# Performance work log

Measured on AMD Instinct MI355X. Metric: run time of the kernel, lower is better.

Reference implementation:

```python
import jax, jax.numpy as jnp
import numpy as np

N_NODES = 100000


def gcn_layer(x, row, col, ew, W, b, n_nodes):
    # PyG GCNConv: add self-loops (weight 1), symmetric normalization
    # deg^{-1/2}[row] * w * deg^{-1/2}[col], linear transform, scatter-add to col.
    loop = jnp.arange(n_nodes, dtype=row.dtype)
    row_f = jnp.concatenate([row, loop])
    col_f = jnp.concatenate([col, loop])
    ew_f = jnp.concatenate([ew, jnp.ones((n_nodes,), dtype=ew.dtype)])
    deg = jax.ops.segment_sum(ew_f, col_f, num_segments=n_nodes)  # [N]
    dinv = jnp.where(deg > 0, jax.lax.rsqrt(deg), 0.0)
    norm = dinv[row_f] * ew_f * dinv[col_f]  # [E+N]
    h = x @ W  # [N, F_out]
    msg = norm[:, None] * h[row_f]  # [E+N, F_out]
    out = jax.ops.segment_sum(msg, col_f, num_segments=n_nodes)
    return out + b


def setup_inputs() -> dict:
    key = jax.random.key(0)
    ks = jax.random.split(key, 6)
    n, e, d_in, d_h = N_NODES, 3200000, 128, 16
    x = jax.random.normal(ks[0], (n, d_in), dtype=jnp.float32)
    edge_index = jax.random.randint(ks[1], (2, e), 0, n, dtype=jnp.int64)
    edge_weight = jax.random.uniform(ks[2], (e,), dtype=jnp.float32)
    W1 = jax.random.normal(ks[3], (d_in, d_h), dtype=jnp.float32) * (1.0 / np.sqrt(d_in))
    b1 = jnp.zeros((d_h,), dtype=jnp.float32)
    W2 = jax.random.normal(ks[4], (d_h, 1), dtype=jnp.float32) * (1.0 / np.sqrt(d_h))
    b2 = jnp.zeros((1,), dtype=jnp.float32)
    return {"x": x, "edge_index": edge_index, "edge_weight": edge_weight,
            "W1": W1, "b1": b1, "W2": W2, "b2": b2}


def reference(x, edge_index, edge_weight, W1, b1, W2, b2):
    row, col = edge_index[0], edge_index[1]
    n = x.shape[0]
    h = gcn_layer(x, row, col, edge_weight, W1, b1, n)
    h = jax.nn.relu(h)
    out = gcn_layer(h, row, col, edge_weight, W2, b2, n)
    return out.squeeze(-1)  # [N]
```

## Files before the change

### kernel.cpp

```cpp
#include <hip/hip_runtime.h>
#include <hip/hip_bf16.h>


#define DH 16
#define BSH 6
#define BNODES 64
#define NB_MAX 1568
#define CHUNK 4096
#define HCHUNK 8192
#define NSLICE 4
#define SE_CAP 768
#define SE2_CAP 1280

#define BFL(u) __uint_as_float((u) << 16)
#define BFH(u) __uint_as_float((u) & 0xFFFF0000u)

typedef unsigned int u32x2 __attribute__((ext_vector_type(2)));

static __device__ __forceinline__ uint2 ntload_u2(const uint2* p) {
    u32x2 v = __builtin_nontemporal_load((const u32x2*)p);
    return make_uint2(v.x, v.y);
}
static __device__ __forceinline__ uint agent_load_u32(const uint* p) {
    return __hip_atomic_load((uint*)p, __ATOMIC_RELAXED, __HIP_MEMORY_SCOPE_AGENT);
}
static __device__ __forceinline__ ushort agent_load_u16(const ushort* p) {
    return __hip_atomic_load((ushort*)p, __ATOMIC_RELAXED, __HIP_MEMORY_SCOPE_AGENT);
}

__global__ __launch_bounds__(256) void k_Ahist(const int* __restrict__ col,
                                               int* __restrict__ gCnt, int E, int NB) {
    __shared__ int lh[NB_MAX];
    const int tid = threadIdx.x;
    for (int i = tid; i < NB; i += 256) lh[i] = 0;
    __syncthreads();
    const int base = blockIdx.x * HCHUNK;
    #pragma unroll
    for (int k = 0; k < 32; ++k) {
        int e = base + tid + 256 * k;
        if (e < E) atomicAdd(&lh[col[e] >> BSH], 1);
    }
    __syncthreads();
    for (int i = tid; i < NB; i += 256) {
        int v = lh[i];
        if (v) atomicAdd(&gCnt[i], v);
    }
}

__global__ __launch_bounds__(1024) void k_Ascan(const int* __restrict__ gCnt,
                                                int* __restrict__ gBase,
                                                int* __restrict__ gCursor,
                                                int NB, int E) {
    __shared__ int s[1024];
    const int t = threadIdx.x;
    const int i0 = 2 * t, i1 = 2 * t + 1;
    int a = (i0 < NB) ? gCnt[i0] : 0;
    int b = (i1 < NB) ? gCnt[i1] : 0;
    int v = a + b;
    s[t] = v;
    __syncthreads();
    for (int off = 1; off < 1024; off <<= 1) {
        int u = (t >= off) ? s[t - off] : 0;
        __syncthreads();
        s[t] += u;
        __syncthreads();
    }
    int ex = s[t] - v;
    if (i0 < NB) { gBase[i0] = ex;     gCursor[i0] = ex; }
    if (i1 < NB) { gBase[i1] = ex + a; gCursor[i1] = ex + a; }
    if (t == 0) gBase[NB] = E;
}

__global__ __launch_bounds__(256) void k_Ascatter(const int* __restrict__ row,
                                                  const int* __restrict__ col,
                                                  const float* __restrict__ ew,
                                                  int* __restrict__ gCursor,
                                                  uint2* __restrict__ edata,
                                                  int E, int NB) {
    __shared__ int lh[NB_MAX];
    __shared__ int lbase[NB_MAX];
    __shared__ int lcur[NB_MAX];
    __shared__ int tsum[256];
    __shared__ unsigned short sbuck[CHUNK];
    __shared__ uint2 stage[CHUNK];
    const int tid = threadIdx.x;
    for (int i = tid; i < NB; i += 256) lh[i] = 0;
    __syncthreads();
    const int base = blockIdx.x * CHUNK;
    int r_[16], c_[16];
    float w_[16];
    #pragma unroll
    for (int k = 0; k < 16; ++k) {
        int e = base + tid + 256 * k;
        bool ok = e < E;
        c_[k] = ok ? col[e] : -1;
        r_[k] = ok ? row[e] : 0;
        w_[k] = ok ? ew[e] : 0.f;
        if (ok) atomicAdd(&lh[c_[k] >> BSH], 1);
    }
    __syncthreads();
    const int t0 = tid * 8;
    int c8[8];
    int mysum = 0;
    #pragma unroll
    for (int k = 0; k < 8; ++k) {
        c8[k] = (t0 + k < NB) ? lh[t0 + k] : 0;
        mysum += c8[k];
    }
    tsum[tid] = mysum;
    __syncthreads();
    for (int off = 1; off < 256; off <<= 1) {
        int u = (tid >= off) ? tsum[tid - off] : 0;
        __syncthreads();
        tsum[tid] += u;
        __syncthreads();
    }
    int p = tsum[tid] - mysum;
    #pragma unroll
    for (int k = 0; k < 8; ++k) {
        if (t0 + k < NB) { lbase[t0 + k] = p; lcur[t0 + k] = p; }
        p += c8[k];
    }
    __syncthreads();
    for (int b = tid; b < NB; b += 256) {
        int cnt = lh[b];
        if (cnt) {
            int g = atomicAdd(&gCursor[b], cnt);
            lh[b] = g - lbase[b];
        }
    }
    __syncthreads();
    #pragma unroll
    for (int k = 0; k < 16; ++k) {
        if (c_[k] >= 0) {
            int b = c_[k] >> BSH;
            unsigned rem = (unsigned)(c_[k] & (BNODES - 1));
            int sp = atomicAdd(&lcur[b], 1);
            stage[sp] = make_uint2((unsigned)r_[k] | (rem << 20), __float_as_uint(w_[k]));
            sbuck[sp] = (unsigned short)b;
        }
    }
    __syncthreads();
    int nE = E - base;
    if (nE > CHUNK) nE = CHUNK;
    for (int j = tid; j < nE; j += 256)
        edata[lh[sbuck[j]] + j] = stage[j];
}

__global__ __launch_bounds__(256) void k_deg(const int* __restrict__ gBase,
                                             const uint2* __restrict__ edata,
                                             float* __restrict__ deg, int N) {
    __shared__ float dg[BNODES];
    const int tid = threadIdx.x;
    if (tid < BNODES) dg[tid] = 0.f;
    __syncthreads();
    const int b = blockIdx.x;
    const int s = gBase[b], e = gBase[b + 1];
    for (int i = s + blockIdx.y * 256 + tid; i < e; i += 512) {
        uint2 ed = ntload_u2(&edata[i]);
        atomicAdd(&dg[ed.x >> 20], __uint_as_float(ed.y));
    }
    __syncthreads();
    int node = (b << BSH) + tid;
    if (tid < BNODES && node < N && dg[tid] != 0.f)
        atomicAdd(&deg[node], dg[tid]);
}

__global__ __launch_bounds__(256) void k_h1(const float* __restrict__ x,
                                            const float* __restrict__ W1,
                                            const float* __restrict__ deg,
                                            float* __restrict__ dinv,
                                            __hip_bfloat16* __restrict__ hdb) {
    __shared__ float Ws[128 * DH];
    __shared__ float xs[16 * 132];
    const int t = threadIdx.x;
    const int node0 = blockIdx.x * 16;
    #pragma unroll
    for (int i = 0; i < 8; ++i) Ws[t + 256 * i] = W1[t + 256 * i];
    const float4* xg = (const float4*)(x + (size_t)node0 * 128);
    #pragma unroll
    for (int it = 0; it < 2; ++it) {
        int idx = t + 256 * it;
        int n = idx >> 5, k4 = idx & 31;
        float4 v = xg[n * 32 + k4];
        *(float4*)(&xs[n * 132 + k4 * 4]) = v;
    }
    __syncthreads();
    const int node = t >> 4, feat = t & 15;
    const float* xr = &xs[node * 132];
    float acc = 0.f;
    #pragma unroll 8
    for (int k = 0; k < 128; ++k) acc += xr[k] * Ws[k * DH + feat];
    const int v = node0 + node;
    const float di = rsqrtf(deg[v] + 1.0f);
    if (feat == 0) dinv[v] = di;
    hdb[(size_t)v * DH + feat] = __float2bfloat16(di * acc);
}

__global__ __launch_bounds__(256) void k_gather1(
    const int* __restrict__ gBase, const uint2* __restrict__ edata,
    const __hip_bfloat16* __restrict__ hdb, float* __restrict__ partial) {
    __shared__ float acc[BNODES][DH + 1];
    __shared__ uint2 se[SE_CAP];
    const int tid = threadIdx.x;
    for (int i = tid; i < BNODES * (DH + 1); i += 256) ((float*)acc)[i] = 0.f;
    const int b = blockIdx.x, sl = blockIdx.y;
    const int s = gBase[b], e = gBase[b + 1];
    const int L = e - s;
    const int per = (L + NSLICE - 1) / NSLICE;
    const int s0 = s + sl * per;
    const int e0 = (s0 + per < e) ? (s0 + per) : e;
    const int g = tid >> 3;
    const int f2 = tid & 7;
    const uint* __restrict__ hp = (const uint*)hdb;

    for (int c0 = s0; c0 < e0; c0 += SE_CAP) {
        const int len = ((e0 - c0) < SE_CAP) ? (e0 - c0) : SE_CAP;
        __syncthreads();
        for (int j = tid; j < len; j += 256) se[j] = ntload_u2(&edata[c0 + j]);
        __syncthreads();
        const int nfull = len & ~255;
        for (int j0 = 0; j0 < nfull; j0 += 256) {
            uint2 ed[8];
            uint hv[8];
            #pragma unroll
            for (int k = 0; k < 8; ++k) ed[k] = se[j0 + g + k * 32];
            #pragma unroll
            for (int k = 0; k < 8; ++k)
                hv[k] = agent_load_u32(&hp[(size_t)(ed[k].x & 0xFFFFFu) * 8 + f2]);
            #pragma unroll
            for (int k = 0; k < 8; ++k) {
                const float w = __uint_as_float(ed[k].y);
                const int rem = ed[k].x >> 20;
                atomicAdd(&acc[rem][2 * f2],     w * BFL(hv[k]));
                atomicAdd(&acc[rem][2 * f2 + 1], w * BFH(hv[k]));
            }
        }
        for (int j = nfull + g; j < len; j += 32) {
            const uint2 ed = se[j];
            const uint hv = agent_load_u32(&hp[(size_t)(ed.x & 0xFFFFFu) * 8 + f2]);
            const float w = __uint_as_float(ed.y);
            const int rem = ed.x >> 20;
            atomicAdd(&acc[rem][2 * f2],     w * BFL(hv));
            atomicAdd(&acc[rem][2 * f2 + 1], w * BFH(hv));
        }
    }
    __syncthreads();
    float* ps = partial + ((size_t)b * NSLICE + sl) * (DH * BNODES);
    for (int i = tid; i < DH * BNODES; i += 256)
        ps[i] = acc[i >> 4][i & 15];
}

__global__ __launch_bounds__(256) void k_fin1(
    const float* __restrict__ partial, const float* __restrict__ dinv,
    const __hip_bfloat16* __restrict__ hdb, const float* __restrict__ b1,
    const float* __restrict__ W2, const float* __restrict__ b2,
    __hip_bfloat16* __restrict__ qb, float* __restrict__ out, int N) {
    __shared__ float acc[BNODES][DH + 1];
    __shared__ float b1s[DH], W2s[DH];
    const int tid = threadIdx.x;
    if (tid < DH) { b1s[tid] = b1[tid]; W2s[tid] = W2[tid]; }
    const int b = blockIdx.x;
    const float* ps = partial + (size_t)b * NSLICE * (DH * BNODES);
    for (int i = tid; i < DH * BNODES; i += 256) {
        float s = 0.f;
        #pragma unroll
        for (int sl = 0; sl < NSLICE; ++sl) s += ps[sl * (DH * BNODES) + i];
        acc[i >> 4][i & 15] = s;
    }
    __syncthreads();
    int node = (b << BSH) + tid;
    if (tid < BNODES && node < N) {
        float dc = dinv[node];
        const __hip_bfloat16* hs = hdb + (size_t)node * DH;
        float t = 0.f;
        #pragma unroll
        for (int f = 0; f < DH; ++f) {
            float hv = __bfloat162float(hs[f]);
            t += fmaxf(dc * (acc[tid][f] + hv) + b1s[f], 0.f) * W2s[f];
        }
        float qq = dc * t;
        qb[node] = __float2bfloat16(qq);
        out[node] = b2[0] + dc * qq;
    }
}

__global__ __launch_bounds__(256) void k_gather2(
    const int* __restrict__ gBase, const uint2* __restrict__ edata,
    const float* __restrict__ dinv, const __hip_bfloat16* __restrict__ qb,
    float* __restrict__ out, int N) {
    __shared__ float a2[BNODES];
    __shared__ uint2 se[SE2_CAP];
    const int tid = threadIdx.x;
    if (tid < BNODES) a2[tid] = 0.f;
    const int b = blockIdx.x;
    const int s = gBase[b], e = gBase[b + 1];
    const int L = e - s;
    const int per = (L + 1) >> 1;
    const int s0 = s + blockIdx.y * per;
    const int e0 = (s0 + per < e) ? (s0 + per) : e;
    const ushort* __restrict__ qp = (const ushort*)qb;

    for (int c0 = s0; c0 < e0; c0 += SE2_CAP) {
        const int len = ((e0 - c0) < SE2_CAP) ? (e0 - c0) : SE2_CAP;
        __syncthreads();
        for (int j = tid; j < len; j += 256) se[j] = ntload_u2(&edata[c0 + j]);
        __syncthreads();
        const int nfull = len & ~1023;
        for (int j0 = 0; j0 < nfull; j0 += 1024) {
            uint2 ed[4];
            uint qv[4];
            #pragma unroll
            for (int k = 0; k < 4; ++k) ed[k] = se[j0 + tid + k * 256];
            #pragma unroll
            for (int k = 0; k < 4; ++k)
                qv[k] = (uint)agent_load_u16(&qp[ed[k].x & 0xFFFFFu]);
            #pragma unroll
            for (int k = 0; k < 4; ++k)
                atomicAdd(&a2[ed[k].x >> 20],
                          __uint_as_float(ed[k].y) * __uint_as_float(qv[k] << 16));
        }
        for (int j = nfull + tid; j < len; j += 256) {
            const uint2 ed = se[j];
            const float q = __uint_as_float((uint)agent_load_u16(&qp[ed.x & 0xFFFFFu]) << 16);
            atomicAdd(&a2[ed.x >> 20], __uint_as_float(ed.y) * q);
        }
    }
    __syncthreads();
    int node = (b << BSH) + tid;
    if (tid < BNODES && node < N && a2[tid] != 0.f)
        atomicAdd(&out[node], dinv[node] * a2[tid]);
}

extern "C" void kernel_launch(void* const* d_in, const int* in_sizes, int n_in,
                              void* d_out, int out_size, void* d_ws, size_t ws_size,
                              hipStream_t stream) {
    const float* x  = (const float*)d_in[0];
    const int*   ei = (const int*)d_in[1];
    const float* ew = (const float*)d_in[2];
    const float* W1 = (const float*)d_in[3];
    const float* b1 = (const float*)d_in[4];
    const float* W2 = (const float*)d_in[5];
    const float* b2 = (const float*)d_in[6];
    float* out = (float*)d_out;

    const int N = in_sizes[0] / 128;
    const int E = in_sizes[2];
    const int* row = ei;
    const int* col = ei + E;
    const int NB = (N + BNODES - 1) >> BSH;
    const int NBp = (NB + 3) & ~3;

    int* gCnt    = (int*)d_ws;
    float* deg   = (float*)(gCnt + NBp);
    int* gBase   = (int*)(deg + N);
    int* gCursor = gBase + NBp;
    float* dinv  = (float*)(gCursor + NBp);
    __hip_bfloat16* hdb = (__hip_bfloat16*)(dinv + N);
    __hip_bfloat16* qb  = hdb + (size_t)16 * N;
    uintptr_t pp = (uintptr_t)(qb + N);
    pp = (pp + 15) & ~(uintptr_t)15;
    float* partial = (float*)pp;
    uintptr_t ep = (uintptr_t)(partial + (size_t)NB * NSLICE * (DH * BNODES));
    ep = (ep + 15) & ~(uintptr_t)15;
    uint2* edata = (uint2*)ep;

    const int hblocks = (E + HCHUNK - 1) / HCHUNK;
    const int sblocks = (E + CHUNK - 1) / CHUNK;

    hipMemsetAsync(gCnt, 0, ((size_t)NBp + N) * sizeof(int), stream);
    k_Ahist<<<hblocks, 256, 0, stream>>>(col, gCnt, E, NB);
    k_Ascan<<<1, 1024, 0, stream>>>(gCnt, gBase, gCursor, NB, E);
    k_Ascatter<<<sblocks, 256, 0, stream>>>(row, col, ew, gCursor, edata, E, NB);
    k_deg<<<dim3(NB, 2), 256, 0, stream>>>(gBase, edata, deg, N);
    k_h1<<<N / 16, 256, 0, stream>>>(x, W1, deg, dinv, hdb);
    k_gather1<<<dim3(NB, NSLICE), 256, 0, stream>>>(gBase, edata, hdb, partial);
    k_fin1<<<NB, 256, 0, stream>>>(partial, dinv, hdb, b1, W2, b2, qb, out, N);
    k_gather2<<<dim3(NB, 2), 256, 0, stream>>>(gBase, edata, dinv, qb, out, N);
}
```

Baseline: 532.5 us.

## Replace random feature gathers with row-bucketed scatter into edge-ordered buffers

Adds a second histogram and scatter that bucket edges by source row and record each edge's slot in the col-sorted order. Source features are then pushed from per-block shared memory into an edge-ordered buffer (he16, qe), so the gather kernels read contiguously instead of doing random per-edge loads of h and q. This adds an extra scatter pass, extra workspace of roughly 32 bytes per edge, and possibly several phases when workspace is limited. A fallback path keeps the old algorithm, with plain loads replacing agent-scope atomic loads.

```diff
diff --git a/kernel.cpp b/kernel.cpp
--- a/kernel.cpp
+++ b/kernel.cpp
@@ -8,9 +8,11 @@
 #define NB_MAX 1568
 #define CHUNK 4096
 #define HCHUNK 8192
-#define NSLICE 4
+#define NSL 2
+#define NSL_FB 4
 #define SE_CAP 768
 #define SE2_CAP 1280
+#define HESLACK 65536
 
 #define BFL(u) __uint_as_float((u) << 16)
 #define BFH(u) __uint_as_float((u) & 0xFFFF0000u)
@@ -21,11 +23,31 @@
     u32x2 v = __builtin_nontemporal_load((const u32x2*)p);
     return make_uint2(v.x, v.y);
 }
-static __device__ __forceinline__ uint agent_load_u32(const uint* p) {
-    return __hip_atomic_load((uint*)p, __ATOMIC_RELAXED, __HIP_MEMORY_SCOPE_AGENT);
-}
-static __device__ __forceinline__ ushort agent_load_u16(const ushort* p) {
-    return __hip_atomic_load((ushort*)p, __ATOMIC_RELAXED, __HIP_MEMORY_SCOPE_AGENT);
+
+
+__global__ __launch_bounds__(256) void k_hist2(const int* __restrict__ row,
+                                               const int* __restrict__ col,
+                                               int* __restrict__ gCnt,
+                                               int* __restrict__ rCnt, int E, int NB) {
+    __shared__ int lc[NB_MAX];
+    __shared__ int lr[NB_MAX];
+    const int tid = threadIdx.x;
+    for (int i = tid; i < NB; i += 256) { lc[i] = 0; lr[i] = 0; }
+    __syncthreads();
+    const int base = blockIdx.x * HCHUNK;
+    #pragma unroll
+    for (int k = 0; k < 32; ++k) {
+        int e = base + tid + 256 * k;
+        if (e < E) {
+            atomicAdd(&lc[col[e] >> BSH], 1);
+            atomicAdd(&lr[row[e] >> BSH], 1);
+        }
+    }
+    __syncthreads();
+    for (int i = tid; i < NB; i += 256) {
+        if (lc[i]) atomicAdd(&gCnt[i], lc[i]);
+        if (lr[i]) atomicAdd(&rCnt[i], lr[i]);
+    }
 }
 
 __global__ __launch_bounds__(256) void k_Ahist(const int* __restrict__ col,
@@ -47,15 +69,15 @@
     }
 }
 
-__global__ __launch_bounds__(1024) void k_Ascan(const int* __restrict__ gCnt,
-                                                int* __restrict__ gBase,
-                                                int* __restrict__ gCursor,
+__global__ __launch_bounds__(1024) void k_Ascan(const int* __restrict__ cnt,
+                                                int* __restrict__ basep,
+                                                int* __restrict__ cursor,
                                                 int NB, int E) {
     __shared__ int s[1024];
     const int t = threadIdx.x;
     const int i0 = 2 * t, i1 = 2 * t + 1;
-    int a = (i0 < NB) ? gCnt[i0] : 0;
-    int b = (i1 < NB) ? gCnt[i1] : 0;
+    int a = (i0 < NB) ? cnt[i0] : 0;
+    int b = (i1 < NB) ? cnt[i1] : 0;
     int v = a + b;
     s[t] = v;
     __syncthreads();
@@ -66,9 +88,9 @@
         __syncthreads();
     }
     int ex = s[t] - v;
-    if (i0 < NB) { gBase[i0] = ex;     gCursor[i0] = ex; }
-    if (i1 < NB) { gBase[i1] = ex + a; gCursor[i1] = ex + a; }
-    if (t == 0) gBase[NB] = E;
+    if (i0 < NB) { basep[i0] = ex;     cursor[i0] = ex; }
+    if (i1 < NB) { basep[i1] = ex + a; cursor[i1] = ex + a; }
+    if (t == 0) basep[NB] = E;
 }
 
 __global__ __launch_bounds__(256) void k_Ascatter(const int* __restrict__ row,
@@ -76,6 +98,7 @@
                                                   const float* __restrict__ ew,
                                                   int* __restrict__ gCursor,
                                                   uint2* __restrict__ edata,
+                                                  int* __restrict__ pos,
                                                   int E, int NB) {
     __shared__ int lh[NB_MAX];
     __shared__ int lbase[NB_MAX];
@@ -138,6 +161,7 @@
             int sp = atomicAdd(&lcur[b], 1);
             stage[sp] = make_uint2((unsigned)r_[k] | (rem << 20), __float_as_uint(w_[k]));
             sbuck[sp] = (unsigned short)b;
+            if (pos != nullptr) pos[base + tid + 256 * k] = lh[b] + sp;
         }
     }
     __syncthreads();
@@ -145,6 +169,80 @@
     if (nE > CHUNK) nE = CHUNK;
     for (int j = tid; j < nE; j += 256)
         edata[lh[sbuck[j]] + j] = stage[j];
+}
+
+__global__ __launch_bounds__(256) void k_Rscatter(const int* __restrict__ row,
+                                                  const int* __restrict__ pos,
+                                                  int* __restrict__ rCursor,
+                                                  uint* __restrict__ rrec,
+                                                  int E, int NB) {
+    __shared__ int lh[NB_MAX];
+    __shared__ int lbase[NB_MAX];
+    __shared__ int lcur[NB_MAX];
+    __shared__ int tsum[256];
+    __shared__ unsigned short sbuck[CHUNK];
+    __shared__ uint stage[CHUNK];
+    const int tid = threadIdx.x;
+    for (int i = tid; i < NB; i += 256) lh[i] = 0;
+    __syncthreads();
+    const int base = blockIdx.x * CHUNK;
+    int r_[16];
+    uint p_[16];
+    #pragma unroll
+    for (int k = 0; k < 16; ++k) {
+        int e = base + tid + 256 * k;
+        bool ok = e < E;
+        r_[k] = ok ? row[e] : -1;
+        p_[k] = ok ? (uint)pos[e] : 0u;
+        if (ok) atomicAdd(&lh[r_[k] >> BSH], 1);
+    }
+    __syncthreads();
+    const int t0 = tid * 8;
+    int c8[8];
+    int mysum = 0;
+    #pragma unroll
+    for (int k = 0; k < 8; ++k) {
+        c8[k] = (t0 + k < NB) ? lh[t0 + k] : 0;
+        mysum += c8[k];
+    }
+    tsum[tid] = mysum;
+    __syncthreads();
+    for (int off = 1; off < 256; off <<= 1) {
+        int u = (tid >= off) ? tsum[tid - off] : 0;
+        __syncthreads();
+        tsum[tid] += u;
+        __syncthreads();
+    }
+    int p = tsum[tid] - mysum;
+    #pragma unroll
+    for (int k = 0; k < 8; ++k) {
+        if (t0 + k < NB) { lbase[t0 + k] = p; lcur[t0 + k] = p; }
+        p += c8[k];
+    }
+    __syncthreads();
+    for (int bb = tid; bb < NB; bb += 256) {
+        int cnt = lh[bb];
+        if (cnt) {
+            int g = atomicAdd(&rCursor[bb], cnt);
+            lh[bb] = g - lbase[bb];
+        }
+    }
+    __syncthreads();
+    #pragma unroll
+    for (int k = 0; k < 16; ++k) {
+        if (r_[k] >= 0) {
+            int bb = r_[k] >> BSH;
+            uint rem = (uint)(r_[k] & (BNODES - 1));
+            int sp = atomicAdd(&lcur[bb], 1);
+            stage[sp] = p_[k] | (rem << 26);
+            sbuck[sp] = (unsigned short)bb;
+        }
+    }
+    __syncthreads();
+    int nE = E - base;
+    if (nE > CHUNK) nE = CHUNK;
+    for (int j = tid; j < nE; j += 256)
+        rrec[lh[sbuck[j]] + j] = stage[j];
 }
 
 __global__ __launch_bounds__(256) void k_deg(const int* __restrict__ gBase,
@@ -197,75 +295,101 @@
     hdb[(size_t)v * DH + feat] = __float2bfloat16(di * acc);
 }
 
-__global__ __launch_bounds__(256) void k_gather1(
+
+__global__ __launch_bounds__(256) void k_hgather(const int* __restrict__ rBase,
+                                                 const uint* __restrict__ rrec,
+                                                 const uint* __restrict__ hdb32,
+                                                 uint4* __restrict__ he16, int N,
+                                                 const int* __restrict__ gBase,
+                                                 int bLo, int bHi, int heCap) {
+    __shared__ uint hs[BNODES * 8];
+    const int tid = threadIdx.x;
+    const int b = blockIdx.x;
+    const int slotLo = gBase[bLo], slotHi = gBase[bHi];
+    const int lim = N * 8 - b * 512;
+    for (int i = tid; i < 512; i += 256)
+        hs[i] = (i < lim) ? hdb32[(size_t)b * 512 + i] : 0u;
+    __syncthreads();
+    const int r0 = rBase[b], r1 = rBase[b + 1];
+    for (int j = r0 + blockIdx.y * 256 + tid; j < r1; j += 512) {
+        uint rec = rrec[j];
+        int p = (int)(rec & 0x03FFFFFFu);
+        if (p >= slotLo && p < slotHi) {
+            int q = p - slotLo;
+            if (q < heCap) {
+                const uint* hr = &hs[(rec >> 26) * 8];
+                he16[(size_t)2 * q]     = make_uint4(hr[0], hr[1], hr[2], hr[3]);
+                he16[(size_t)2 * q + 1] = make_uint4(hr[4], hr[5], hr[6], hr[7]);
+            }
+        }
+    }
+}
+
+__global__ __launch_bounds__(256) void k_gather1_p(
     const int* __restrict__ gBase, const uint2* __restrict__ edata,
-    const __hip_bfloat16* __restrict__ hdb, float* __restrict__ partial) {
+    const uint4* __restrict__ he16, float* __restrict__ partial,
+    int bLo, int heCap) {
     __shared__ float acc[BNODES][DH + 1];
-    __shared__ uint2 se[SE_CAP];
     const int tid = threadIdx.x;
     for (int i = tid; i < BNODES * (DH + 1); i += 256) ((float*)acc)[i] = 0.f;
-    const int b = blockIdx.x, sl = blockIdx.y;
+    __syncthreads();
+    const int b = bLo + blockIdx.x, sl = blockIdx.y;
+    const int slotLo = gBase[bLo];
     const int s = gBase[b], e = gBase[b + 1];
     const int L = e - s;
-    const int per = (L + NSLICE - 1) / NSLICE;
+    const int per = (L + NSL - 1) / NSL;
     const int s0 = s + sl * per;
     const int e0 = (s0 + per < e) ? (s0 + per) : e;
-    const int g = tid >> 3;
-    const int f2 = tid & 7;
-    const uint* __restrict__ hp = (const uint*)hdb;
-
-    for (int c0 = s0; c0 < e0; c0 += SE_CAP) {
-        const int len = ((e0 - c0) < SE_CAP) ? (e0 - c0) : SE_CAP;
-        __syncthreads();
-        for (int j = tid; j < len; j += 256) se[j] = ntload_u2(&edata[c0 + j]);
-        __syncthreads();
-        const int nfull = len & ~255;
-        for (int j0 = 0; j0 < nfull; j0 += 256) {
-            uint2 ed[8];
-            uint hv[8];
-            #pragma unroll
-            for (int k = 0; k < 8; ++k) ed[k] = se[j0 + g + k * 32];
-            #pragma unroll
-            for (int k = 0; k < 8; ++k)
-                hv[k] = agent_load_u32(&hp[(size_t)(ed[k].x & 0xFFFFFu) * 8 + f2]);
-            #pragma unroll
-            for (int k = 0; k < 8; ++k) {
-                const float w = __uint_as_float(ed[k].y);
-                const int rem = ed[k].x >> 20;
-                atomicAdd(&acc[rem][2 * f2],     w * BFL(hv[k]));
-                atomicAdd(&acc[rem][2 * f2 + 1], w * BFH(hv[k]));
-            }
-        }
-        for (int j = nfull + g; j < len; j += 32) {
-            const uint2 ed = se[j];
-            const uint hv = agent_load_u32(&hp[(size_t)(ed.x & 0xFFFFFu) * 8 + f2]);
-            const float w = __uint_as_float(ed.y);
-            const int rem = ed.x >> 20;
-            atomicAdd(&acc[rem][2 * f2],     w * BFL(hv));
-            atomicAdd(&acc[rem][2 * f2 + 1], w * BFH(hv));
-        }
-    }
-    __syncthreads();
-    float* ps = partial + ((size_t)b * NSLICE + sl) * (DH * BNODES);
+    const int hf = tid & 1, f0 = hf * 8;
+    for (int jb = s0; jb < e0; jb += 256) {
+        const int j0 = jb + (tid >> 1);
+        const int j1 = j0 + 128;
+        const bool v0 = (j0 < e0) && (j0 - slotLo < heCap);
+        const bool v1 = (j1 < e0) && (j1 - slotLo < heCap);
+        uint4 h0 = v0 ? he16[(size_t)2 * (j0 - slotLo) + hf] : make_uint4(0, 0, 0, 0);
+        uint4 h1 = v1 ? he16[(size_t)2 * (j1 - slotLo) + hf] : make_uint4(0, 0, 0, 0);
+        uint2 d0 = v0 ? edata[j0] : make_uint2(0u, 0u);
+        uint2 d1 = v1 ? edata[j1] : make_uint2(0u, 0u);
+        {
+            const float w = __uint_as_float(d0.y);
+            float* a = &acc[d0.x >> 20][f0];
+            atomicAdd(a + 0, w * BFL(h0.x)); atomicAdd(a + 1, w * BFH(h0.x));
+            atomicAdd(a + 2, w * BFL(h0.y)); atomicAdd(a + 3, w * BFH(h0.y));
+            atomicAdd(a + 4, w * BFL(h0.z)); atomicAdd(a + 5, w * BFH(h0.z));
+            atomicAdd(a + 6, w * BFL(h0.w)); atomicAdd(a + 7, w * BFH(h0.w));
+        }
+        {
+            const float w = __uint_as_float(d1.y);
+            float* a = &acc[d1.x >> 20][f0];
+            atomicAdd(a + 0, w * BFL(h1.x)); atomicAdd(a + 1, w * BFH(h1.x));
+            atomicAdd(a + 2, w * BFL(h1.y)); atomicAdd(a + 3, w * BFH(h1.y));
+            atomicAdd(a + 4, w * BFL(h1.z)); atomicAdd(a + 5, w * BFH(h1.z));
+            atomicAdd(a + 6, w * BFL(h1.w)); atomicAdd(a + 7, w * BFH(h1.w));
+        }
+    }
+    __syncthreads();
+    float* ps = partial + ((size_t)b * NSL + sl) * (DH * BNODES);
     for (int i = tid; i < DH * BNODES; i += 256)
         ps[i] = acc[i >> 4][i & 15];
 }
 
-__global__ __launch_bounds__(256) void k_fin1(
+__global__ __launch_bounds__(256) void k_fin1_p(
     const float* __restrict__ partial, const float* __restrict__ dinv,
     const __hip_bfloat16* __restrict__ hdb, const float* __restrict__ b1,
     const float* __restrict__ W2, const float* __restrict__ b2,
-    __hip_bfloat16* __restrict__ qb, float* __restrict__ out, int N) {
+    const int* __restrict__ rBase, const uint* __restrict__ rrec,
+    __hip_bfloat16* __restrict__ qe, float* __restrict__ out, int N) {
     __shared__ float acc[BNODES][DH + 1];
     __shared__ float b1s[DH], W2s[DH];
+    __shared__ __hip_bfloat16 qls[BNODES];
     const int tid = threadIdx.x;
     if (tid < DH) { b1s[tid] = b1[tid]; W2s[tid] = W2[tid]; }
     const int b = blockIdx.x;
-    const float* ps = partial + (size_t)b * NSLICE * (DH * BNODES);
+    const float* ps = partial + (size_t)b * NSL * (DH * BNODES);
     for (int i = tid; i < DH * BNODES; i += 256) {
         float s = 0.f;
         #pragma unroll
-        for (int sl = 0; sl < NSLICE; ++sl) s += ps[sl * (DH * BNODES) + i];
+        for (int sl = 0; sl < NSL; ++sl) s += ps[sl * (DH * BNODES) + i];
         acc[i >> 4][i & 15] = s;
     }
     __syncthreads();
@@ -280,12 +404,137 @@
             t += fmaxf(dc * (acc[tid][f] + hv) + b1s[f], 0.f) * W2s[f];
         }
         float qq = dc * t;
+        qls[tid] = __float2bfloat16(qq);
+        out[node] = b2[0] + dc * qq;
+    } else if (tid < BNODES) {
+        qls[tid] = __float2bfloat16(0.f);
+    }
+    __syncthreads();
+    const int r0 = rBase[b], r1 = rBase[b + 1];
+    for (int j = r0 + tid; j < r1; j += 256) {
+        uint rec = rrec[j];
+        qe[rec & 0x03FFFFFFu] = qls[rec >> 26];
+    }
+}
+
+__global__ __launch_bounds__(256) void k_gather2_p(
+    const int* __restrict__ gBase, const uint2* __restrict__ edata,
+    const float* __restrict__ dinv, const __hip_bfloat16* __restrict__ qe,
+    float* __restrict__ out, int N) {
+    __shared__ float a2[BNODES];
+    const int tid = threadIdx.x;
+    if (tid < BNODES) a2[tid] = 0.f;
+    __syncthreads();
+    const int b = blockIdx.x;
+    const int s = gBase[b], e = gBase[b + 1];
+    const int L = e - s;
+    const int per = (L + 1) >> 1;
+    const int s0 = s + blockIdx.y * per;
+    const int e0 = (s0 + per < e) ? (s0 + per) : e;
+    for (int i = s0 + tid; i < e0; i += 512) {
+        const int i1 = i + 256;
+        uint2 d0 = edata[i];
+        uint2 d1 = (i1 < e0) ? edata[i1] : make_uint2(0u, 0u);
+        float q0 = __bfloat162float(qe[i]);
+        float q1 = (i1 < e0) ? __bfloat162float(qe[i1]) : 0.f;
+        atomicAdd(&a2[d0.x >> 20], __uint_as_float(d0.y) * q0);
+        atomicAdd(&a2[d1.x >> 20], __uint_as_float(d1.y) * q1);
+    }
+    __syncthreads();
+    int node = (b << BSH) + tid;
+    if (tid < BNODES && node < N && a2[tid] != 0.f)
+        atomicAdd(&out[node], dinv[node] * a2[tid]);
+}
+
+
+__global__ __launch_bounds__(256) void k_gather1_fb(
+    const int* __restrict__ gBase, const uint2* __restrict__ edata,
+    const __hip_bfloat16* __restrict__ hdb, float* __restrict__ partial) {
+    __shared__ float acc[BNODES][DH + 1];
+    __shared__ uint2 se[SE_CAP];
+    const int tid = threadIdx.x;
+    for (int i = tid; i < BNODES * (DH + 1); i += 256) ((float*)acc)[i] = 0.f;
+    const int b = blockIdx.x, sl = blockIdx.y;
+    const int s = gBase[b], e = gBase[b + 1];
+    const int L = e - s;
+    const int per = (L + NSL_FB - 1) / NSL_FB;
+    const int s0 = s + sl * per;
+    const int e0 = (s0 + per < e) ? (s0 + per) : e;
+    const int g = tid >> 3;
+    const int f2 = tid & 7;
+    const uint* __restrict__ hp = (const uint*)hdb;
+    for (int c0 = s0; c0 < e0; c0 += SE_CAP) {
+        const int len = ((e0 - c0) < SE_CAP) ? (e0 - c0) : SE_CAP;
+        __syncthreads();
+        for (int j = tid; j < len; j += 256) se[j] = ntload_u2(&edata[c0 + j]);
+        __syncthreads();
+        const int nfull = len & ~255;
+        for (int j0 = 0; j0 < nfull; j0 += 256) {
+            uint2 ed[8];
+            uint hv[8];
+            #pragma unroll
+            for (int k = 0; k < 8; ++k) ed[k] = se[j0 + g + k * 32];
+            #pragma unroll
+            for (int k = 0; k < 8; ++k)
+                hv[k] = hp[(size_t)(ed[k].x & 0xFFFFFu) * 8 + f2];
+            #pragma unroll
+            for (int k = 0; k < 8; ++k) {
+                const float w = __uint_as_float(ed[k].y);
+                const int rem = ed[k].x >> 20;
+                atomicAdd(&acc[rem][2 * f2],     w * BFL(hv[k]));
+                atomicAdd(&acc[rem][2 * f2 + 1], w * BFH(hv[k]));
+            }
+        }
+        for (int j = nfull + g; j < len; j += 32) {
+            const uint2 ed = se[j];
+            const uint hv = hp[(size_t)(ed.x & 0xFFFFFu) * 8 + f2];
+            const float w = __uint_as_float(ed.y);
+            const int rem = ed.x >> 20;
+            atomicAdd(&acc[rem][2 * f2],     w * BFL(hv));
+            atomicAdd(&acc[rem][2 * f2 + 1], w * BFH(hv));
+        }
+    }
+    __syncthreads();
+    float* ps = partial + ((size_t)b * NSL_FB + sl) * (DH * BNODES);
+    for (int i = tid; i < DH * BNODES; i += 256)
+        ps[i] = acc[i >> 4][i & 15];
+}
+
+__global__ __launch_bounds__(256) void k_fin1_fb(
+    const float* __restrict__ partial, const float* __restrict__ dinv,
+    const __hip_bfloat16* __restrict__ hdb, const float* __restrict__ b1,
+    const float* __restrict__ W2, const float* __restrict__ b2,
+    __hip_bfloat16* __restrict__ qb, float* __restrict__ out, int N) {
+    __shared__ float acc[BNODES][DH + 1];
+    __shared__ float b1s[DH], W2s[DH];
+    const int tid = threadIdx.x;
+    if (tid < DH) { b1s[tid] = b1[tid]; W2s[tid] = W2[tid]; }
+    const int b = blockIdx.x;
+    const float* ps = partial + (size_t)b * NSL_FB * (DH * BNODES);
+    for (int i = tid; i < DH * BNODES; i += 256) {
+        float s = 0.f;
+        #pragma unroll
+        for (int sl = 0; sl < NSL_FB; ++sl) s += ps[sl * (DH * BNODES) + i];
+        acc[i >> 4][i & 15] = s;
+    }
+    __syncthreads();
+    int node = (b << BSH) + tid;
+    if (tid < BNODES && node < N) {
+        float dc = dinv[node];
+        const __hip_bfloat16* hs = hdb + (size_t)node * DH;
+        float t = 0.f;
+        #pragma unroll
+        for (int f = 0; f < DH; ++f) {
+            float hv = __bfloat162float(hs[f]);
+            t += fmaxf(dc * (acc[tid][f] + hv) + b1s[f], 0.f) * W2s[f];
+        }
+        float qq = dc * t;
         qb[node] = __float2bfloat16(qq);
         out[node] = b2[0] + dc * qq;
     }
 }
 
-__global__ __launch_bounds__(256) void k_gather2(
+__global__ __launch_bounds__(256) void k_gather2_fb(
     const int* __restrict__ gBase, const uint2* __restrict__ edata,
     const float* __restrict__ dinv, const __hip_bfloat16* __restrict__ qb,
     float* __restrict__ out, int N) {
@@ -300,29 +549,14 @@
     const int s0 = s + blockIdx.y * per;
     const int e0 = (s0 + per < e) ? (s0 + per) : e;
     const ushort* __restrict__ qp = (const ushort*)qb;
-
     for (int c0 = s0; c0 < e0; c0 += SE2_CAP) {
         const int len = ((e0 - c0) < SE2_CAP) ? (e0 - c0) : SE2_CAP;
         __syncthreads();
         for (int j = tid; j < len; j += 256) se[j] = ntload_u2(&edata[c0 + j]);
         __syncthreads();
-        const int nfull = len & ~1023;
-        for (int j0 = 0; j0 < nfull; j0 += 1024) {
-            uint2 ed[4];
-            uint qv[4];
-            #pragma unroll
-            for (int k = 0; k < 4; ++k) ed[k] = se[j0 + tid + k * 256];
-            #pragma unroll
-            for (int k = 0; k < 4; ++k)
-                qv[k] = (uint)agent_load_u16(&qp[ed[k].x & 0xFFFFFu]);
-            #pragma unroll
-            for (int k = 0; k < 4; ++k)
-                atomicAdd(&a2[ed[k].x >> 20],
-                          __uint_as_float(ed[k].y) * __uint_as_float(qv[k] << 16));
-        }
-        for (int j = nfull + tid; j < len; j += 256) {
+        for (int j = tid; j < len; j += 256) {
             const uint2 ed = se[j];
-            const float q = __uint_as_float((uint)agent_load_u16(&qp[ed.x & 0xFFFFFu]) << 16);
+            const float q = __uint_as_float((uint)qp[ed.x & 0xFFFFFu] << 16);
             atomicAdd(&a2[ed.x >> 20], __uint_as_float(ed.y) * q);
         }
     }
@@ -331,6 +565,7 @@
     if (tid < BNODES && node < N && a2[tid] != 0.f)
         atomicAdd(&out[node], dinv[node] * a2[tid]);
 }
+
 
 extern "C" void kernel_launch(void* const* d_in, const int* in_sizes, int n_in,
                               void* d_out, int out_size, void* d_ws, size_t ws_size,
@@ -349,32 +584,82 @@
     const int* row = ei;
     const int* col = ei + E;
     const int NB = (N + BNODES - 1) >> BSH;
-    const int NBp = (NB + 3) & ~3;
-
-    int* gCnt    = (int*)d_ws;
-    float* deg   = (float*)(gCnt + NBp);
-    int* gBase   = (int*)(deg + N);
-    int* gCursor = gBase + NBp;
-    float* dinv  = (float*)(gCursor + NBp);
-    __hip_bfloat16* hdb = (__hip_bfloat16*)(dinv + N);
-    __hip_bfloat16* qb  = hdb + (size_t)16 * N;
-    uintptr_t pp = (uintptr_t)(qb + N);
-    pp = (pp + 15) & ~(uintptr_t)15;
-    float* partial = (float*)pp;
-    uintptr_t ep = (uintptr_t)(partial + (size_t)NB * NSLICE * (DH * BNODES));
-    ep = (ep + 15) & ~(uintptr_t)15;
-    uint2* edata = (uint2*)ep;
 
     const int hblocks = (E + HCHUNK - 1) / HCHUNK;
     const int sblocks = (E + CHUNK - 1) / CHUNK;
 
-    hipMemsetAsync(gCnt, 0, ((size_t)NBp + N) * sizeof(int), stream);
-    k_Ahist<<<hblocks, 256, 0, stream>>>(col, gCnt, E, NB);
-    k_Ascan<<<1, 1024, 0, stream>>>(gCnt, gBase, gCursor, NB, E);
-    k_Ascatter<<<sblocks, 256, 0, stream>>>(row, col, ew, gCursor, edata, E, NB);
-    k_deg<<<dim3(NB, 2), 256, 0, stream>>>(gBase, edata, deg, N);
-    k_h1<<<N / 16, 256, 0, stream>>>(x, W1, deg, dinv, hdb);
-    k_gather1<<<dim3(NB, NSLICE), 256, 0, stream>>>(gBase, edata, hdb, partial);
-    k_fin1<<<NB, 256, 0, stream>>>(partial, dinv, hdb, b1, W2, b2, qb, out, N);
-    k_gather2<<<dim3(NB, 2), 256, 0, stream>>>(gBase, edata, dinv, qb, out, N);
-}
+    const int NBp = NB_MAX;
+    char* base = (char*)d_ws;
+    size_t off = 0;
+    int*   gCnt    = (int*)(base + off);   off += (size_t)NBp * 4;
+    int*   rCnt    = (int*)(base + off);   off += (size_t)NBp * 4;
+    float* deg     = (float*)(base + off); off += (size_t)N * 4;
+    int*   gBase   = (int*)(base + off);   off += (size_t)NBp * 4;
+    int*   rBase   = (int*)(base + off);   off += (size_t)NBp * 4;
+    int*   gCursor = (int*)(base + off);   off += (size_t)NBp * 4;
+    int*   rCursor = (int*)(base + off);   off += (size_t)NBp * 4;
+    float* dinv    = (float*)(base + off); off += (size_t)N * 4;
+    __hip_bfloat16* hdb = (__hip_bfloat16*)(base + off); off += (size_t)16 * N * 2;
+    __hip_bfloat16* qe  = (__hip_bfloat16*)(base + off); off += (size_t)E * 2;
+    uint*  rrec    = (uint*)(base + off);  off += (size_t)E * 4;
+    float* partial = (float*)(base + off); off += (size_t)NB * NSL * (DH * BNODES) * 4;
+    uint2* edata   = (uint2*)(base + off); off += (size_t)E * 8;
+    int*   pos     = (int*)(base + off);
+    uint4* he16    = (uint4*)(base + off);
+    const size_t base_need = off;
+
+    int nph = 0;
+    int heCap = 0;
+    const int cands[4] = {1, 2, 4, 8};
+    for (int c = 0; c < 4; ++c) {
+        int cap = E / cands[c] + HESLACK;
+        if (base_need + (size_t)cap * 32 <= ws_size) { nph = cands[c]; heCap = cap; break; }
+    }
+
+    if (nph > 0) {
+        hipMemsetAsync(gCnt, 0, ((size_t)2 * NBp + N) * sizeof(int), stream);
+        k_hist2<<<hblocks, 256, 0, stream>>>(row, col, gCnt, rCnt, E, NB);
+        k_Ascan<<<1, 1024, 0, stream>>>(gCnt, gBase, gCursor, NB, E);
+        k_Ascan<<<1, 1024, 0, stream>>>(rCnt, rBase, rCursor, NB, E);
+        k_Ascatter<<<sblocks, 256, 0, stream>>>(row, col, ew, gCursor, edata, pos, E, NB);
+        k_Rscatter<<<sblocks, 256, 0, stream>>>(row, pos, rCursor, rrec, E, NB);
+        k_deg<<<dim3(NB, 2), 256, 0, stream>>>(gBase, edata, deg, N);
+        k_h1<<<N / 16, 256, 0, stream>>>(x, W1, deg, dinv, hdb);
+        for (int ph = 0; ph < nph; ++ph) {
+            int bLo = (int)((long long)NB * ph / nph);
+            int bHi = (int)((long long)NB * (ph + 1) / nph);
+            k_hgather<<<dim3(NB, 2), 256, 0, stream>>>(rBase, rrec, (const uint*)hdb,
+                                                       he16, N, gBase, bLo, bHi, heCap);
+            k_gather1_p<<<dim3(bHi - bLo, NSL), 256, 0, stream>>>(gBase, edata, he16,
+                                                                  partial, bLo, heCap);
+        }
+        k_fin1_p<<<NB, 256, 0, stream>>>(partial, dinv, hdb, b1, W2, b2,
+                                         rBase, rrec, qe, out, N);
+        k_gather2_p<<<dim3(NB, 2), 256, 0, stream>>>(gBase, edata, dinv, qe, out, N);
+    } else {
+        const int NBf = (NB + 3) & ~3;
+        int* fgCnt    = (int*)d_ws;
+        float* fdeg   = (float*)(fgCnt + NBf);
+        int* fgBase   = (int*)(fdeg + N);
+        int* fgCursor = fgBase + NBf;
+        float* fdinv  = (float*)(fgCursor + NBf);
+        __hip_bfloat16* fhdb = (__hip_bfloat16*)(fdinv + N);
+        __hip_bfloat16* fqb  = fhdb + (size_t)16 * N;
+        uintptr_t pp = (uintptr_t)(fqb + N);
+        pp = (pp + 15) & ~(uintptr_t)15;
+        float* fpartial = (float*)pp;
+        uintptr_t ep = (uintptr_t)(fpartial + (size_t)NB * NSL_FB * (DH * BNODES));
+        ep = (ep + 15) & ~(uintptr_t)15;
+        uint2* fedata = (uint2*)ep;
+
+        hipMemsetAsync(fgCnt, 0, ((size_t)NBf + N) * sizeof(int), stream);
+        k_Ahist<<<hblocks, 256, 0, stream>>>(col, fgCnt, E, NB);
+        k_Ascan<<<1, 1024, 0, stream>>>(fgCnt, fgBase, fgCursor, NB, E);
+        k_Ascatter<<<sblocks, 256, 0, stream>>>(row, col, ew, fgCursor, fedata, nullptr, E, NB);
+        k_deg<<<dim3(NB, 2), 256, 0, stream>>>(fgBase, fedata, fdeg, N);
+        k_h1<<<N / 16, 256, 0, stream>>>(x, W1, fdeg, fdinv, fhdb);
+        k_gather1_fb<<<dim3(NB, NSL_FB), 256, 0, stream>>>(fgBase, fedata, fhdb, fpartial);
+        k_fin1_fb<<<NB, 256, 0, stream>>>(fpartial, fdinv, fhdb, b1, W2, b2, fqb, out, N);
+        k_gather2_fb<<<dim3(NB, 2), 256, 0, stream>>>(fgBase, fedata, fdinv, fqb, out, N);
+    }
+}
```

Result: slower. 740.0 us (+39.0%).

## Push layer-2 node values into per-edge order to make gather2 contiguous

Applied to the files above, without the earlier changes.

Adds a second bucketing of edges by source row, with a position map back into the col-sorted edge array. After computing q per node, k_fin1q scatters each source node's q value to the CSC-ordered slots of its outgoing edges, so gather2 reads q contiguously instead of through random 2-byte loads. This exchanges a random gather for an extra histogram, scan and scatter pass plus a random 2-byte scatter write and about 10 bytes of extra workspace per edge. It also replaces the agent-scope atomic loads of h in gather1 with plain loads.

```diff
diff --git a/kernel.cpp b/kernel.cpp
--- a/kernel.cpp
+++ b/kernel.cpp
@@ -10,7 +10,7 @@
 #define HCHUNK 8192
 #define NSLICE 4
 #define SE_CAP 768
-#define SE2_CAP 1280
+#define CH2 1024
 
 #define BFL(u) __uint_as_float((u) << 16)
 #define BFH(u) __uint_as_float((u) & 0xFFFF0000u)
@@ -21,41 +21,41 @@
     u32x2 v = __builtin_nontemporal_load((const u32x2*)p);
     return make_uint2(v.x, v.y);
 }
-static __device__ __forceinline__ uint agent_load_u32(const uint* p) {
-    return __hip_atomic_load((uint*)p, __ATOMIC_RELAXED, __HIP_MEMORY_SCOPE_AGENT);
-}
-static __device__ __forceinline__ ushort agent_load_u16(const ushort* p) {
-    return __hip_atomic_load((ushort*)p, __ATOMIC_RELAXED, __HIP_MEMORY_SCOPE_AGENT);
-}
-
-__global__ __launch_bounds__(256) void k_Ahist(const int* __restrict__ col,
-                                               int* __restrict__ gCnt, int E, int NB) {
-    __shared__ int lh[NB_MAX];
-    const int tid = threadIdx.x;
-    for (int i = tid; i < NB; i += 256) lh[i] = 0;
+
+__global__ __launch_bounds__(256) void k_hist2(const int* __restrict__ row,
+                                               const int* __restrict__ col,
+                                               int* __restrict__ gCnt,
+                                               int* __restrict__ rCnt, int E, int NB) {
+    __shared__ int lc[NB_MAX];
+    __shared__ int lr[NB_MAX];
+    const int tid = threadIdx.x;
+    for (int i = tid; i < NB; i += 256) { lc[i] = 0; lr[i] = 0; }
     __syncthreads();
     const int base = blockIdx.x * HCHUNK;
     #pragma unroll
     for (int k = 0; k < 32; ++k) {
         int e = base + tid + 256 * k;
-        if (e < E) atomicAdd(&lh[col[e] >> BSH], 1);
+        if (e < E) {
+            atomicAdd(&lc[col[e] >> BSH], 1);
+            atomicAdd(&lr[row[e] >> BSH], 1);
+        }
     }
     __syncthreads();
     for (int i = tid; i < NB; i += 256) {
-        int v = lh[i];
-        if (v) atomicAdd(&gCnt[i], v);
-    }
-}
-
-__global__ __launch_bounds__(1024) void k_Ascan(const int* __restrict__ gCnt,
-                                                int* __restrict__ gBase,
-                                                int* __restrict__ gCursor,
+        if (lc[i]) atomicAdd(&gCnt[i], lc[i]);
+        if (lr[i]) atomicAdd(&rCnt[i], lr[i]);
+    }
+}
+
+__global__ __launch_bounds__(1024) void k_Ascan(const int* __restrict__ cnt,
+                                                int* __restrict__ basep,
+                                                int* __restrict__ cursor,
                                                 int NB, int E) {
     __shared__ int s[1024];
     const int t = threadIdx.x;
     const int i0 = 2 * t, i1 = 2 * t + 1;
-    int a = (i0 < NB) ? gCnt[i0] : 0;
-    int b = (i1 < NB) ? gCnt[i1] : 0;
+    int a = (i0 < NB) ? cnt[i0] : 0;
+    int b = (i1 < NB) ? cnt[i1] : 0;
     int v = a + b;
     s[t] = v;
     __syncthreads();
@@ -66,9 +66,9 @@
         __syncthreads();
     }
     int ex = s[t] - v;
-    if (i0 < NB) { gBase[i0] = ex;     gCursor[i0] = ex; }
-    if (i1 < NB) { gBase[i1] = ex + a; gCursor[i1] = ex + a; }
-    if (t == 0) gBase[NB] = E;
+    if (i0 < NB) { basep[i0] = ex;     cursor[i0] = ex; }
+    if (i1 < NB) { basep[i1] = ex + a; cursor[i1] = ex + a; }
+    if (t == 0) basep[NB] = E;
 }
 
 __global__ __launch_bounds__(256) void k_Ascatter(const int* __restrict__ row,
@@ -76,6 +76,7 @@
                                                   const float* __restrict__ ew,
                                                   int* __restrict__ gCursor,
                                                   uint2* __restrict__ edata,
+                                                  int* __restrict__ pos,
                                                   int E, int NB) {
     __shared__ int lh[NB_MAX];
     __shared__ int lbase[NB_MAX];
@@ -138,6 +139,7 @@
             int sp = atomicAdd(&lcur[b], 1);
             stage[sp] = make_uint2((unsigned)r_[k] | (rem << 20), __float_as_uint(w_[k]));
             sbuck[sp] = (unsigned short)b;
+            pos[base + tid + 256 * k] = lh[b] + sp;
         }
     }
     __syncthreads();
@@ -145,6 +147,80 @@
     if (nE > CHUNK) nE = CHUNK;
     for (int j = tid; j < nE; j += 256)
         edata[lh[sbuck[j]] + j] = stage[j];
+}
+
+__global__ __launch_bounds__(256) void k_Rscatter(const int* __restrict__ row,
+                                                  const int* __restrict__ pos,
+                                                  int* __restrict__ rCursor,
+                                                  uint* __restrict__ rrec,
+                                                  int E, int NB) {
+    __shared__ int lh[NB_MAX];
+    __shared__ int lbase[NB_MAX];
+    __shared__ int lcur[NB_MAX];
+    __shared__ int tsum[256];
+    __shared__ unsigned short sbuck[CHUNK];
+    __shared__ uint stage[CHUNK];
+    const int tid = threadIdx.x;
+    for (int i = tid; i < NB; i += 256) lh[i] = 0;
+    __syncthreads();
+    const int base = blockIdx.x * CHUNK;
+    int r_[16];
+    uint p_[16];
+    #pragma unroll
+    for (int k = 0; k < 16; ++k) {
+        int e = base + tid + 256 * k;
+        bool ok = e < E;
+        r_[k] = ok ? row[e] : -1;
+        p_[k] = ok ? (uint)pos[e] : 0u;
+        if (ok) atomicAdd(&lh[r_[k] >> BSH], 1);
+    }
+    __syncthreads();
+    const int t0 = tid * 8;
+    int c8[8];
+    int mysum = 0;
+    #pragma unroll
+    for (int k = 0; k < 8; ++k) {
+        c8[k] = (t0 + k < NB) ? lh[t0 + k] : 0;
+        mysum += c8[k];
+    }
+    tsum[tid] = mysum;
+    __syncthreads();
+    for (int off = 1; off < 256; off <<= 1) {
+        int u = (tid >= off) ? tsum[tid - off] : 0;
+        __syncthreads();
+        tsum[tid] += u;
+        __syncthreads();
+    }
+    int p = tsum[tid] - mysum;
+    #pragma unroll
+    for (int k = 0; k < 8; ++k) {
+        if (t0 + k < NB) { lbase[t0 + k] = p; lcur[t0 + k] = p; }
+        p += c8[k];
+    }
+    __syncthreads();
+    for (int bb = tid; bb < NB; bb += 256) {
+        int cnt = lh[bb];
+        if (cnt) {
+            int g = atomicAdd(&rCursor[bb], cnt);
+            lh[bb] = g - lbase[bb];
+        }
+    }
+    __syncthreads();
+    #pragma unroll
+    for (int k = 0; k < 16; ++k) {
+        if (r_[k] >= 0) {
+            int bb = r_[k] >> BSH;
+            uint rem = (uint)(r_[k] & (BNODES - 1));
+            int sp = atomicAdd(&lcur[bb], 1);
+            stage[sp] = p_[k] | (rem << 26);
+            sbuck[sp] = (unsigned short)bb;
+        }
+    }
+    __syncthreads();
+    int nE = E - base;
+    if (nE > CHUNK) nE = CHUNK;
+    for (int j = tid; j < nE; j += 256)
+        rrec[lh[sbuck[j]] + j] = stage[j];
 }
 
 __global__ __launch_bounds__(256) void k_deg(const int* __restrict__ gBase,
@@ -227,7 +303,7 @@
             for (int k = 0; k < 8; ++k) ed[k] = se[j0 + g + k * 32];
             #pragma unroll
             for (int k = 0; k < 8; ++k)
-                hv[k] = agent_load_u32(&hp[(size_t)(ed[k].x & 0xFFFFFu) * 8 + f2]);
+                hv[k] = hp[(size_t)(ed[k].x & 0xFFFFFu) * 8 + f2];
             #pragma unroll
             for (int k = 0; k < 8; ++k) {
                 const float w = __uint_as_float(ed[k].y);
@@ -238,7 +314,7 @@
         }
         for (int j = nfull + g; j < len; j += 32) {
             const uint2 ed = se[j];
-            const uint hv = agent_load_u32(&hp[(size_t)(ed.x & 0xFFFFFu) * 8 + f2]);
+            const uint hv = hp[(size_t)(ed.x & 0xFFFFFu) * 8 + f2];
             const float w = __uint_as_float(ed.y);
             const int rem = ed.x >> 20;
             atomicAdd(&acc[rem][2 * f2],     w * BFL(hv));
@@ -251,13 +327,15 @@
         ps[i] = acc[i >> 4][i & 15];
 }
 
-__global__ __launch_bounds__(256) void k_fin1(
+__global__ __launch_bounds__(256) void k_fin1q(
     const float* __restrict__ partial, const float* __restrict__ dinv,
     const __hip_bfloat16* __restrict__ hdb, const float* __restrict__ b1,
     const float* __restrict__ W2, const float* __restrict__ b2,
-    __hip_bfloat16* __restrict__ qb, float* __restrict__ out, int N) {
+    const int* __restrict__ rBase, const uint* __restrict__ rrec,
+    __hip_bfloat16* __restrict__ qe, float* __restrict__ out, int N) {
     __shared__ float acc[BNODES][DH + 1];
     __shared__ float b1s[DH], W2s[DH];
+    __shared__ __hip_bfloat16 qls[BNODES];
     const int tid = threadIdx.x;
     if (tid < DH) { b1s[tid] = b1[tid]; W2s[tid] = W2[tid]; }
     const int b = blockIdx.x;
@@ -280,17 +358,26 @@
             t += fmaxf(dc * (acc[tid][f] + hv) + b1s[f], 0.f) * W2s[f];
         }
         float qq = dc * t;
-        qb[node] = __float2bfloat16(qq);
+        qls[tid] = __float2bfloat16(qq);
         out[node] = b2[0] + dc * qq;
-    }
-}
-
-__global__ __launch_bounds__(256) void k_gather2(
+    } else if (tid < BNODES) {
+        qls[tid] = __float2bfloat16(0.f);
+    }
+    __syncthreads();
+    const int r0 = rBase[b], r1 = rBase[b + 1];
+    for (int j = r0 + tid; j < r1; j += 256) {
+        uint rec = rrec[j];
+        qe[rec & 0x03FFFFFFu] = qls[rec >> 26];
+    }
+}
+
+__global__ __launch_bounds__(256) void k_gather2q(
     const int* __restrict__ gBase, const uint2* __restrict__ edata,
-    const float* __restrict__ dinv, const __hip_bfloat16* __restrict__ qb,
+    const float* __restrict__ dinv, const __hip_bfloat16* __restrict__ qe,
     float* __restrict__ out, int N) {
     __shared__ float a2[BNODES];
-    __shared__ uint2 se[SE2_CAP];
+    __shared__ uint2 se[CH2];
+    __shared__ ushort sq[CH2];
     const int tid = threadIdx.x;
     if (tid < BNODES) a2[tid] = 0.f;
     const int b = blockIdx.x;
@@ -299,31 +386,22 @@
     const int per = (L + 1) >> 1;
     const int s0 = s + blockIdx.y * per;
     const int e0 = (s0 + per < e) ? (s0 + per) : e;
-    const ushort* __restrict__ qp = (const ushort*)qb;
-
-    for (int c0 = s0; c0 < e0; c0 += SE2_CAP) {
-        const int len = ((e0 - c0) < SE2_CAP) ? (e0 - c0) : SE2_CAP;
-        __syncthreads();
-        for (int j = tid; j < len; j += 256) se[j] = ntload_u2(&edata[c0 + j]);
-        __syncthreads();
-        const int nfull = len & ~1023;
-        for (int j0 = 0; j0 < nfull; j0 += 1024) {
-            uint2 ed[4];
-            uint qv[4];
-            #pragma unroll
-            for (int k = 0; k < 4; ++k) ed[k] = se[j0 + tid + k * 256];
-            #pragma unroll
-            for (int k = 0; k < 4; ++k)
-                qv[k] = (uint)agent_load_u16(&qp[ed[k].x & 0xFFFFFu]);
-            #pragma unroll
-            for (int k = 0; k < 4; ++k)
-                atomicAdd(&a2[ed[k].x >> 20],
-                          __uint_as_float(ed[k].y) * __uint_as_float(qv[k] << 16));
-        }
-        for (int j = nfull + tid; j < len; j += 256) {
-            const uint2 ed = se[j];
-            const float q = __uint_as_float((uint)agent_load_u16(&qp[ed.x & 0xFFFFFu]) << 16);
-            atomicAdd(&a2[ed.x >> 20], __uint_as_float(ed.y) * q);
+    const ushort* __restrict__ qp = (const ushort*)qe;
+
+    for (int c0 = s0; c0 < e0; c0 += CH2) {
+        const int len = ((e0 - c0) < CH2) ? (e0 - c0) : CH2;
+        __syncthreads();
+        for (int i = tid; i < len; i += 256) se[i] = ntload_u2(&edata[c0 + i]);
+        for (int i = tid; i < len; i += 256) sq[i] = qp[c0 + i];
+        __syncthreads();
+        #pragma unroll
+        for (int k = 0; k < CH2 / 256; ++k) {
+            const int idx = tid + k * 256;
+            if (idx < len) {
+                const uint2 d = se[idx];
+                const float q = __uint_as_float((uint)sq[idx] << 16);
+                atomicAdd(&a2[d.x >> 20], __uint_as_float(d.y) * q);
+            }
         }
     }
     __syncthreads();
@@ -349,32 +427,43 @@
     const int* row = ei;
     const int* col = ei + E;
     const int NB = (N + BNODES - 1) >> BSH;
-    const int NBp = (NB + 3) & ~3;
-
-    int* gCnt    = (int*)d_ws;
-    float* deg   = (float*)(gCnt + NBp);
-    int* gBase   = (int*)(deg + N);
-    int* gCursor = gBase + NBp;
-    float* dinv  = (float*)(gCursor + NBp);
-    __hip_bfloat16* hdb = (__hip_bfloat16*)(dinv + N);
-    __hip_bfloat16* qb  = hdb + (size_t)16 * N;
-    uintptr_t pp = (uintptr_t)(qb + N);
-    pp = (pp + 15) & ~(uintptr_t)15;
-    float* partial = (float*)pp;
-    uintptr_t ep = (uintptr_t)(partial + (size_t)NB * NSLICE * (DH * BNODES));
-    ep = (ep + 15) & ~(uintptr_t)15;
-    uint2* edata = (uint2*)ep;
+    const int NBp = NB_MAX;
 
     const int hblocks = (E + HCHUNK - 1) / HCHUNK;
     const int sblocks = (E + CHUNK - 1) / CHUNK;
 
-    hipMemsetAsync(gCnt, 0, ((size_t)NBp + N) * sizeof(int), stream);
-    k_Ahist<<<hblocks, 256, 0, stream>>>(col, gCnt, E, NB);
+    char* base = (char*)d_ws;
+    size_t off = 0;
+    #define ALLOC(ptr_t, name, bytes) \
+        ptr_t name = (ptr_t)(base + off); off = (off + (size_t)(bytes) + 255) & ~(size_t)255;
+    ALLOC(int*,   gCnt,    (size_t)NBp * 4)
+    ALLOC(int*,   rCnt,    (size_t)NBp * 4)
+    ALLOC(float*, deg,     (size_t)N * 4)
+    ALLOC(int*,   gBase,   (size_t)NBp * 4)
+    ALLOC(int*,   rBase,   (size_t)NBp * 4)
+    ALLOC(int*,   gCursor, (size_t)NBp * 4)
+    ALLOC(int*,   rCursor, (size_t)NBp * 4)
+    ALLOC(float*, dinv,    (size_t)N * 4)
+    ALLOC(__hip_bfloat16*, hdb, (size_t)16 * N * 2)
+    ALLOC(__hip_bfloat16*, qe,  (size_t)E * 2)
+    ALLOC(int*,   pos,     (size_t)E * 4)
+    ALLOC(uint*,  rrec,    (size_t)E * 4)
+    ALLOC(float*, partial, (size_t)NB * NSLICE * (DH * BNODES) * 4)
+    ALLOC(uint2*, edata,   (size_t)E * 8)
+    #undef ALLOC
+
+    hipMemsetAsync(gCnt, 0, ((size_t)NBp) * sizeof(int), stream);
+    hipMemsetAsync(rCnt, 0, ((size_t)NBp) * sizeof(int), stream);
+    hipMemsetAsync(deg,  0, ((size_t)N) * sizeof(float), stream);
+    k_hist2<<<hblocks, 256, 0, stream>>>(row, col, gCnt, rCnt, E, NB);
     k_Ascan<<<1, 1024, 0, stream>>>(gCnt, gBase, gCursor, NB, E);
-    k_Ascatter<<<sblocks, 256, 0, stream>>>(row, col, ew, gCursor, edata, E, NB);
+    k_Ascan<<<1, 1024, 0, stream>>>(rCnt, rBase, rCursor, NB, E);
+    k_Ascatter<<<sblocks, 256, 0, stream>>>(row, col, ew, gCursor, edata, pos, E, NB);
+    k_Rscatter<<<sblocks, 256, 0, stream>>>(row, pos, rCursor, rrec, E, NB);
     k_deg<<<dim3(NB, 2), 256, 0, stream>>>(gBase, edata, deg, N);
     k_h1<<<N / 16, 256, 0, stream>>>(x, W1, deg, dinv, hdb);
     k_gather1<<<dim3(NB, NSLICE), 256, 0, stream>>>(gBase, edata, hdb, partial);
-    k_fin1<<<NB, 256, 0, stream>>>(partial, dinv, hdb, b1, W2, b2, qb, out, N);
-    k_gather2<<<dim3(NB, 2), 256, 0, stream>>>(gBase, edata, dinv, qb, out, N);
-}
+    k_fin1q<<<NB, 256, 0, stream>>>(partial, dinv, hdb, b1, W2, b2,
+                                    rBase, rrec, qe, out, N);
+    k_gather2q<<<dim3(NB, 2), 256, 0, stream>>>(gBase, edata, dinv, qe, out, N);
+}
```

Result: slower. 635.2 us (+19.3%).
